# Kernel optimization log

Measured on AMD Instinct MI355X. Metric: run time of the kernel, lower is better.

Reference implementation:

```python
import jax, jax.numpy as jnp
import numpy as np

N_NODES = 100000
N_EDGES = 1600000
D = 32            # d_v = d_e = d_g = 32
LATENT = 32
IN_FEAT = 3 * D   # nodes + received-edge agg + globals
OUT_FEAT = 32


def setup_inputs() -> dict:
    key = jax.random.key(0)
    ks = jax.random.split(key, 8)
    node_attr = jax.random.normal(ks[0], (N_NODES, D), dtype=jnp.float32)
    edge_index = jax.random.randint(ks[1], (2, N_EDGES), 0, N_NODES, dtype=jnp.int64)
    edge_attr = jax.random.normal(ks[2], (N_EDGES, D), dtype=jnp.float32)
    global_attr = jax.random.normal(ks[3], (1, D), dtype=jnp.float32)
    W1 = jax.random.normal(ks[4], (IN_FEAT, LATENT), dtype=jnp.float32) * (1.0 / np.sqrt(IN_FEAT))
    b1 = jnp.zeros((LATENT,), dtype=jnp.float32)
    W2 = jax.random.normal(ks[5], (LATENT, OUT_FEAT), dtype=jnp.float32) * (1.0 / np.sqrt(LATENT))
    b2 = jnp.zeros((OUT_FEAT,), dtype=jnp.float32)
    return {"node_attr": node_attr, "edge_index": edge_index, "edge_attr": edge_attr,
            "global_attr": global_attr, "W1": W1, "b1": b1, "W2": W2, "b2": b2}


def reference(node_attr, edge_index, edge_attr, global_attr, W1, b1, W2, b2):
    receivers = edge_index[1]
    # scatter_add of edge features by receiver index -> [N, d_e]
    agg_received = jax.ops.segment_sum(edge_attr, receivers, num_segments=N_NODES)
    # broadcast global attr to all nodes -> [N, d_g]
    g = jnp.broadcast_to(global_attr, (N_NODES, global_attr.shape[1]))
    collected = jnp.concatenate([node_attr, agg_received, g], axis=-1)  # [N, 3d]
    h = jax.nn.relu(collected @ W1 + b1)
    return h @ W2 + b2
```

## Files before the change

### kernel.cpp

```cpp
#include <hip/hip_runtime.h>

#define N_NODES 100000
#define N_EDGES 1600000
#define D 32
#define NB 64
#define K_BUCKETS 1563
#define CAP 1280
#define CHUNK 8192
#define PART_BLOCKS 196
#define BINS_PAD 2048
#define CSTRIDE 16

__global__ __launch_bounds__(256) void partition_kernel(
    const int* __restrict__ receivers,
    int* __restrict__ cursor,
    unsigned int* __restrict__ slab)
{
    __shared__ int sHist[BINS_PAD];
    __shared__ int sStart[BINS_PAD];
    __shared__ int sCur[BINS_PAD];
    __shared__ int sTmp[256];
    __shared__ unsigned int sPairs[CHUNK];
    __shared__ unsigned short sBinOf[CHUNK];

    const int tid = threadIdx.x;
    const int base = blockIdx.x * CHUNK;
    const int n = min(CHUNK, N_EDGES - base);

    for (int i = tid; i < BINS_PAD; i += 256) sHist[i] = 0;
    __syncthreads();

    for (int s = 0; s < CHUNK / 256; ++s) {
        int idx = s * 256 + tid;
        if (idx < n) atomicAdd(&sHist[receivers[base + idx] >> 6], 1);
    }
    __syncthreads();

    int loc[8];
    int s = 0;
    #pragma unroll
    for (int i = 0; i < 8; ++i) {
        int v = sHist[tid * 8 + i];
        loc[i] = s;
        s += v;
    }
    sTmp[tid] = s;
    __syncthreads();
    for (int off = 1; off < 256; off <<= 1) {
        int x = sTmp[tid];
        int add = (tid >= off) ? sTmp[tid - off] : 0;
        __syncthreads();
        sTmp[tid] = x + add;
        __syncthreads();
    }
    int excl = sTmp[tid] - s;
    #pragma unroll
    for (int i = 0; i < 8; ++i) {
        int e = excl + loc[i];
        sStart[tid * 8 + i] = e;
        sCur[tid * 8 + i] = e;
    }
    __syncthreads();

    for (int s2 = 0; s2 < CHUNK / 256; ++s2) {
        int idx = s2 * 256 + tid;
        if (idx < n) {
            int r = receivers[base + idx];
            int key = r >> 6;
            int slot = atomicAdd(&sCur[key], 1);
            sPairs[slot] = ((unsigned int)(r & (NB - 1)) << 24) |
                           (unsigned int)(base + idx);
            sBinOf[slot] = (unsigned short)key;
        }
    }
    __syncthreads();

    for (int k = tid; k < K_BUCKETS; k += 256) {
        int c = sHist[k];
        int g = c ? atomicAdd(&cursor[k * CSTRIDE], c) : 0;
        sCur[k] = g - sStart[k];
    }
    __syncthreads();

    for (int idx = tid; idx < n; idx += 256) {
        int k = sBinOf[idx];
        int pos = sCur[k] + idx;
        if ((unsigned)pos < CAP) slab[(size_t)k * CAP + pos] = sPairs[idx];
    }
}

__global__ __launch_bounds__(256) void fused_kernel(
    const float* __restrict__ node_attr,
    const float* __restrict__ edge_attr,
    const unsigned int* __restrict__ slab,
    const int* __restrict__ cursor,
    const float* __restrict__ gattr,
    const float* __restrict__ W1,
    const float* __restrict__ b1,
    const float* __restrict__ W2,
    const float* __restrict__ b2,
    float* __restrict__ out)
{
    __shared__ float sW1n[1024];
    __shared__ float sW1a[1024];
    __shared__ float sW2[1024];
    __shared__ float sBase[32];
    __shared__ float sB2[32];
    __shared__ float sAgg[NB * 36];
    __shared__ float sH[NB * 36];
    __shared__ unsigned int sSorted[CAP];
    __shared__ int sCnt[NB];
    __shared__ int sStart2[NB];
    __shared__ int sCur2[NB];

    const int tid = threadIdx.x;
    for (int i = tid; i < 1024; i += 256) {
        sW1n[i] = W1[i];
        sW1a[i] = W1[1024 + i];
        sW2[i]  = W2[i];
    }
    if (tid < 32) {
        float acc = b1[tid];
        for (int k = 0; k < 32; ++k) acc += gattr[k] * W1[(64 + k) * 32 + tid];
        sBase[tid] = acc;
        sB2[tid] = b2[tid];
    }
    if (tid < NB) sCnt[tid] = 0;
    __syncthreads();

    const int b = blockIdx.x;
    const int count = min(cursor[b * CSTRIDE], CAP);
    const unsigned int* myslab = slab + (size_t)b * CAP;

    unsigned int pr[(CAP + 255) / 256];
    int np = 0;
    for (int i = tid; i < count; i += 256) {
        unsigned int p = myslab[i];
        pr[np++] = p;
        atomicAdd(&sCnt[p >> 24], 1);
    }
    __syncthreads();

    if (tid < 64) {
        int c = sCnt[tid];
        int v = c;
        #pragma unroll
        for (int off = 1; off < 64; off <<= 1) {
            int y = __shfl_up(v, off, 64);
            if (tid >= off) v += y;
        }
        sStart2[tid] = v - c;
        sCur2[tid] = v - c;
    }
    __syncthreads();

    for (int j = 0; j < np; ++j) {
        unsigned int p = pr[j];
        int slot = atomicAdd(&sCur2[p >> 24], 1);
        sSorted[slot] = p & 0xFFFFFFu;
    }
    __syncthreads();

    const int g = tid >> 2;
    const int part = tid & 3;
    const int st = sStart2[g];
    const int cn = sCnt[g];

    float a[8];
    #pragma unroll
    for (int j = 0; j < 8; ++j) a[j] = 0.0f;

    int j = 0;
    for (; j + 1 < cn; j += 2) {
        int e0 = (int)sSorted[st + j];
        int e1 = (int)sSorted[st + j + 1];
        const float* r0 = edge_attr + (size_t)e0 * D + part * 8;
        const float* r1 = edge_attr + (size_t)e1 * D + part * 8;
        float4 u0 = *(const float4*)(r0);
        float4 u1 = *(const float4*)(r0 + 4);
        float4 w0 = *(const float4*)(r1);
        float4 w1 = *(const float4*)(r1 + 4);
        a[0] += u0.x + w0.x; a[1] += u0.y + w0.y;
        a[2] += u0.z + w0.z; a[3] += u0.w + w0.w;
        a[4] += u1.x + w1.x; a[5] += u1.y + w1.y;
        a[6] += u1.z + w1.z; a[7] += u1.w + w1.w;
    }
    if (j < cn) {
        int e0 = (int)sSorted[st + j];
        const float* r0 = edge_attr + (size_t)e0 * D + part * 8;
        float4 u0 = *(const float4*)(r0);
        float4 u1 = *(const float4*)(r0 + 4);
        a[0] += u0.x; a[1] += u0.y; a[2] += u0.z; a[3] += u0.w;
        a[4] += u1.x; a[5] += u1.y; a[6] += u1.z; a[7] += u1.w;
    }
    float* dst = &sAgg[g * 36 + part * 8];
    *(float4*)(dst)     = make_float4(a[0], a[1], a[2], a[3]);
    *(float4*)(dst + 4) = make_float4(a[4], a[5], a[6], a[7]);
    __syncthreads();

    const int node = b * NB + g;
    const bool valid = (node < N_NODES);
    const int node_c = valid ? node : (N_NODES - 1);
    const int jb = part * 8;

    float h[8];
    #pragma unroll
    for (int jj = 0; jj < 8; ++jj) h[jj] = sBase[jb + jj];

    const float4* np4 = (const float4*)(node_attr + (size_t)node_c * D);
    #pragma unroll
    for (int q0 = 0; q0 < 8; ++q0) {
        float4 xv = np4[q0];
        float xk[4] = {xv.x, xv.y, xv.z, xv.w};
        #pragma unroll
        for (int kk = 0; kk < 4; ++kk) {
            int k = 4 * q0 + kk;
            float4 w0 = *(const float4*)&sW1n[k * 32 + jb];
            float4 w1 = *(const float4*)&sW1n[k * 32 + jb + 4];
            h[0] += xk[kk] * w0.x; h[1] += xk[kk] * w0.y;
            h[2] += xk[kk] * w0.z; h[3] += xk[kk] * w0.w;
            h[4] += xk[kk] * w1.x; h[5] += xk[kk] * w1.y;
            h[6] += xk[kk] * w1.z; h[7] += xk[kk] * w1.w;
        }
    }
    #pragma unroll 8
    for (int k = 0; k < 32; ++k) {
        float ak = sAgg[g * 36 + k];
        float4 w0 = *(const float4*)&sW1a[k * 32 + jb];
        float4 w1 = *(const float4*)&sW1a[k * 32 + jb + 4];
        h[0] += ak * w0.x; h[1] += ak * w0.y;
        h[2] += ak * w0.z; h[3] += ak * w0.w;
        h[4] += ak * w1.x; h[5] += ak * w1.y;
        h[6] += ak * w1.z; h[7] += ak * w1.w;
    }
    {
        float* hd = &sH[g * 36 + jb];
        #pragma unroll
        for (int jj = 0; jj < 8; ++jj) hd[jj] = fmaxf(h[jj], 0.0f);
    }
    __syncthreads();

    float o[8];
    #pragma unroll
    for (int jj = 0; jj < 8; ++jj) o[jj] = sB2[jb + jj];
    #pragma unroll 8
    for (int k = 0; k < 32; ++k) {
        float hk = sH[g * 36 + k];
        float4 w0 = *(const float4*)&sW2[k * 32 + jb];
        float4 w1 = *(const float4*)&sW2[k * 32 + jb + 4];
        o[0] += hk * w0.x; o[1] += hk * w0.y;
        o[2] += hk * w0.z; o[3] += hk * w0.w;
        o[4] += hk * w1.x; o[5] += hk * w1.y;
        o[6] += hk * w1.z; o[7] += hk * w1.w;
    }

    if (valid) {
        float4* op4 = (float4*)(out + (size_t)node * D + jb);
        op4[0] = make_float4(o[0], o[1], o[2], o[3]);
        op4[1] = make_float4(o[4], o[5], o[6], o[7]);
    }
}

extern "C" void kernel_launch(void* const* d_in, const int* in_sizes, int n_in,
                              void* d_out, int out_size, void* d_ws, size_t ws_size,
                              hipStream_t stream) {
    const float* node_attr  = (const float*)d_in[0];
    const int*   edge_index = (const int*)d_in[1];
    const float* edge_attr  = (const float*)d_in[2];
    const float* gattr      = (const float*)d_in[3];
    const float* W1         = (const float*)d_in[4];
    const float* b1         = (const float*)d_in[5];
    const float* W2         = (const float*)d_in[6];
    const float* b2         = (const float*)d_in[7];
    float* out = (float*)d_out;

    const int* receivers = edge_index + N_EDGES;

    int* cursor = (int*)d_ws;
    unsigned int* slab =
        (unsigned int*)d_ws + (size_t)BINS_PAD * CSTRIDE;

    hipMemsetAsync(cursor, 0, (size_t)BINS_PAD * CSTRIDE * sizeof(int), stream);

    partition_kernel<<<PART_BLOCKS, 256, 0, stream>>>(receivers, cursor, slab);

    fused_kernel<<<K_BUCKETS, 256, 0, stream>>>(
        node_attr, edge_attr, slab, cursor,
        gattr, W1, b1, W2, b2, out);
}
```

Measured before the change: 365.6 us.

## Restructure partition kernel to scatter directly and widen gather unroll

The partition kernel now uses 512 threads per block and chunks of 4096 edges. Receivers are kept in registers instead of a shared-memory pairs buffer, and the block scan uses wave shuffles. Each edge is written straight to its global slab slot after reserving space with the global cursor atomic, so the local staging pass and the final copy-out loop go away. The fused kernel gets a fixed-count unrolled slab load and a 4-way unrolled edge-attribute gather to expose more memory-level parallelism. The trade-off is that slab writes are less coalesced, and the extra registers may lower occupancy.

```diff
diff --git a/kernel.cpp b/kernel.cpp
--- a/kernel.cpp
+++ b/kernel.cpp
@@ -6,12 +6,15 @@
 #define NB 64
 #define K_BUCKETS 1563
 #define CAP 1280
-#define CHUNK 8192
-#define PART_BLOCKS 196
+#define CHUNK 4096
+#define PB 512
+#define EPT (CHUNK / PB)
+#define PART_BLOCKS 391
 #define BINS_PAD 2048
 #define CSTRIDE 16
-
-__global__ __launch_bounds__(256) void partition_kernel(
+#define NPASS ((CAP + 255) / 256)
+
+__global__ __launch_bounds__(512) void partition_kernel(
     const int* __restrict__ receivers,
     int* __restrict__ cursor,
     unsigned int* __restrict__ slab)
@@ -19,73 +22,71 @@
     __shared__ int sHist[BINS_PAD];
     __shared__ int sStart[BINS_PAD];
     __shared__ int sCur[BINS_PAD];
-    __shared__ int sTmp[256];
-    __shared__ unsigned int sPairs[CHUNK];
-    __shared__ unsigned short sBinOf[CHUNK];
+    __shared__ int sWs[16];
 
     const int tid = threadIdx.x;
     const int base = blockIdx.x * CHUNK;
-    const int n = min(CHUNK, N_EDGES - base);
-
-    for (int i = tid; i < BINS_PAD; i += 256) sHist[i] = 0;
-    __syncthreads();
-
-    for (int s = 0; s < CHUNK / 256; ++s) {
-        int idx = s * 256 + tid;
-        if (idx < n) atomicAdd(&sHist[receivers[base + idx] >> 6], 1);
-    }
-    __syncthreads();
-
-    int loc[8];
-    int s = 0;
-    #pragma unroll
-    for (int i = 0; i < 8; ++i) {
-        int v = sHist[tid * 8 + i];
-        loc[i] = s;
-        s += v;
-    }
-    sTmp[tid] = s;
-    __syncthreads();
-    for (int off = 1; off < 256; off <<= 1) {
-        int x = sTmp[tid];
-        int add = (tid >= off) ? sTmp[tid - off] : 0;
-        __syncthreads();
-        sTmp[tid] = x + add;
-        __syncthreads();
-    }
-    int excl = sTmp[tid] - s;
-    #pragma unroll
-    for (int i = 0; i < 8; ++i) {
+    const int nrem = N_EDGES - base;
+
+    for (int i = tid; i < BINS_PAD; i += PB) sHist[i] = 0;
+    __syncthreads();
+
+    int rv[EPT];
+    #pragma unroll
+    for (int s = 0; s < EPT; ++s) {
+        int idx = s * PB + tid;
+        rv[s] = (idx < nrem) ? receivers[base + idx] : -1;
+        if (rv[s] >= 0) atomicAdd(&sHist[rv[s] >> 6], 1);
+    }
+    __syncthreads();
+
+    int loc[4];
+    int ssum = 0;
+    #pragma unroll
+    for (int i = 0; i < 4; ++i) {
+        int v = sHist[tid * 4 + i];
+        loc[i] = ssum;
+        ssum += v;
+    }
+    int inc = ssum;
+    #pragma unroll
+    for (int off = 1; off < 64; off <<= 1) {
+        int y = __shfl_up(inc, off, 64);
+        if ((tid & 63) >= off) inc += y;
+    }
+    const int wave = tid >> 6;
+    if ((tid & 63) == 63) sWs[wave] = inc;
+    __syncthreads();
+    int wbase = 0;
+    for (int w = 0; w < wave; ++w) wbase += sWs[w];
+    int excl = wbase + inc - ssum;
+    #pragma unroll
+    for (int i = 0; i < 4; ++i) {
         int e = excl + loc[i];
-        sStart[tid * 8 + i] = e;
-        sCur[tid * 8 + i] = e;
-    }
-    __syncthreads();
-
-    for (int s2 = 0; s2 < CHUNK / 256; ++s2) {
-        int idx = s2 * 256 + tid;
-        if (idx < n) {
-            int r = receivers[base + idx];
+        sStart[tid * 4 + i] = e;
+        sCur[tid * 4 + i] = e;
+    }
+    __syncthreads();
+
+    for (int k = tid; k < K_BUCKETS; k += PB) {
+        int c = sHist[k];
+        int g = c ? atomicAdd(&cursor[k * CSTRIDE], c) : 0;
+        sHist[k] = g - sStart[k];
+    }
+    __syncthreads();
+
+    #pragma unroll
+    for (int s = 0; s < EPT; ++s) {
+        int r = rv[s];
+        if (r >= 0) {
             int key = r >> 6;
             int slot = atomicAdd(&sCur[key], 1);
-            sPairs[slot] = ((unsigned int)(r & (NB - 1)) << 24) |
-                           (unsigned int)(base + idx);
-            sBinOf[slot] = (unsigned short)key;
-        }
-    }
-    __syncthreads();
-
-    for (int k = tid; k < K_BUCKETS; k += 256) {
-        int c = sHist[k];
-        int g = c ? atomicAdd(&cursor[k * CSTRIDE], c) : 0;
-        sCur[k] = g - sStart[k];
-    }
-    __syncthreads();
-
-    for (int idx = tid; idx < n; idx += 256) {
-        int k = sBinOf[idx];
-        int pos = sCur[k] + idx;
-        if ((unsigned)pos < CAP) slab[(size_t)k * CAP + pos] = sPairs[idx];
+            int pos = sHist[key] + slot;
+            if ((unsigned)pos < CAP)
+                slab[(size_t)key * CAP + pos] =
+                    ((unsigned int)(r & (NB - 1)) << 24) |
+                    (unsigned int)(base + s * PB + tid);
+        }
     }
 }
 
@@ -132,12 +133,16 @@
     const int count = min(cursor[b * CSTRIDE], CAP);
     const unsigned int* myslab = slab + (size_t)b * CAP;
 
-    unsigned int pr[(CAP + 255) / 256];
-    int np = 0;
-    for (int i = tid; i < count; i += 256) {
-        unsigned int p = myslab[i];
-        pr[np++] = p;
-        atomicAdd(&sCnt[p >> 24], 1);
+    unsigned int pr[NPASS];
+    #pragma unroll
+    for (int it = 0; it < NPASS; ++it) {
+        int i = it * 256 + tid;
+        unsigned int p = 0xFFFFFFFFu;
+        if (i < count) {
+            p = myslab[i];
+            atomicAdd(&sCnt[p >> 24], 1);
+        }
+        pr[it] = p;
     }
     __syncthreads();
 
@@ -154,10 +159,13 @@
     }
     __syncthreads();
 
-    for (int j = 0; j < np; ++j) {
-        unsigned int p = pr[j];
-        int slot = atomicAdd(&sCur2[p >> 24], 1);
-        sSorted[slot] = p & 0xFFFFFFu;
+    #pragma unroll
+    for (int it = 0; it < NPASS; ++it) {
+        unsigned int p = pr[it];
+        if (p != 0xFFFFFFFFu) {
+            int slot = atomicAdd(&sCur2[p >> 24], 1);
+            sSorted[slot] = p & 0xFFFFFFu;
+        }
     }
     __syncthreads();
 
@@ -168,24 +176,36 @@
 
     float a[8];
     #pragma unroll
-    for (int j = 0; j < 8; ++j) a[j] = 0.0f;
+    for (int jj = 0; jj < 8; ++jj) a[jj] = 0.0f;
 
     int j = 0;
-    for (; j + 1 < cn; j += 2) {
+    for (; j + 3 < cn; j += 4) {
         int e0 = (int)sSorted[st + j];
         int e1 = (int)sSorted[st + j + 1];
+        int e2 = (int)sSorted[st + j + 2];
+        int e3 = (int)sSorted[st + j + 3];
         const float* r0 = edge_attr + (size_t)e0 * D + part * 8;
         const float* r1 = edge_attr + (size_t)e1 * D + part * 8;
+        const float* r2 = edge_attr + (size_t)e2 * D + part * 8;
+        const float* r3 = edge_attr + (size_t)e3 * D + part * 8;
         float4 u0 = *(const float4*)(r0);
         float4 u1 = *(const float4*)(r0 + 4);
-        float4 w0 = *(const float4*)(r1);
-        float4 w1 = *(const float4*)(r1 + 4);
-        a[0] += u0.x + w0.x; a[1] += u0.y + w0.y;
-        a[2] += u0.z + w0.z; a[3] += u0.w + w0.w;
-        a[4] += u1.x + w1.x; a[5] += u1.y + w1.y;
-        a[6] += u1.z + w1.z; a[7] += u1.w + w1.w;
-    }
-    if (j < cn) {
+        float4 v0 = *(const float4*)(r1);
+        float4 v1 = *(const float4*)(r1 + 4);
+        float4 w0 = *(const float4*)(r2);
+        float4 w1 = *(const float4*)(r2 + 4);
+        float4 x0 = *(const float4*)(r3);
+        float4 x1 = *(const float4*)(r3 + 4);
+        a[0] += (u0.x + v0.x) + (w0.x + x0.x);
+        a[1] += (u0.y + v0.y) + (w0.y + x0.y);
+        a[2] += (u0.z + v0.z) + (w0.z + x0.z);
+        a[3] += (u0.w + v0.w) + (w0.w + x0.w);
+        a[4] += (u1.x + v1.x) + (w1.x + x1.x);
+        a[5] += (u1.y + v1.y) + (w1.y + x1.y);
+        a[6] += (u1.z + v1.z) + (w1.z + x1.z);
+        a[7] += (u1.w + v1.w) + (w1.w + x1.w);
+    }
+    for (; j < cn; ++j) {
         int e0 = (int)sSorted[st + j];
         const float* r0 = edge_attr + (size_t)e0 * D + part * 8;
         float4 u0 = *(const float4*)(r0);
@@ -282,7 +302,7 @@
 
     hipMemsetAsync(cursor, 0, (size_t)BINS_PAD * CSTRIDE * sizeof(int), stream);
 
-    partition_kernel<<<PART_BLOCKS, 256, 0, stream>>>(receivers, cursor, slab);
+    partition_kernel<<<PART_BLOCKS, PB, 0, stream>>>(receivers, cursor, slab);
 
     fused_kernel<<<K_BUCKETS, 256, 0, stream>>>(
         node_attr, edge_attr, slab, cursor,
```

New measurement: 368.0 us. No clear change (+0.7%).
